# Kernel optimization log

Measured on AMD Instinct MI355X. Metric: run time of the kernel, lower is better.

The kernel has to match this reference:

```python
import jax, jax.numpy as jnp
import numpy as np

B, C, N, K, COUT = 4, 64, 8192, 16, 64
EPS = 1e-5  # BatchNorm1d default eps


def setup_inputs() -> dict:
    key = jax.random.key(0)
    k1, k2, k3 = jax.random.split(key, 3)
    x = jax.random.normal(k1, (B, C, N), dtype=jnp.float32)
    coords = jax.random.normal(k2, (B, 3, N), dtype=jnp.float32)
    # Linear(2C -> COUT) params
    W = jax.random.normal(k3, (2 * C, COUT), dtype=jnp.float32) * (1.0 / np.sqrt(2 * C))
    b = jnp.zeros((COUT,), dtype=jnp.float32)
    # BatchNorm1d affine params (train-mode batch stats, as in torch default)
    gamma = jnp.ones((COUT,), dtype=jnp.float32)
    beta = jnp.zeros((COUT,), dtype=jnp.float32)
    return {"x": x, "coords": coords, "W": W, "b": b, "gamma": gamma, "beta": beta}


def reference(x, coords, W, b, gamma, beta):
    k = min(K, max(N - 1, 1))
    # --- kNN in coordinate space (squared distances give same ordering as cdist) ---
    ct = jnp.swapaxes(coords, 1, 2)                      # (B, N, 3)
    sq = jnp.sum(ct * ct, axis=-1)                       # (B, N)
    d2 = sq[:, :, None] + sq[:, None, :] - 2.0 * jnp.einsum('bnd,bmd->bnm', ct, ct)
    _, idx = jax.lax.top_k(-d2, k + 1)                   # smallest k+1 distances
    idx = idx[:, :, 1:]                                  # drop self -> (B, N, k)
    # --- gather neighbor features ---
    xt = jnp.swapaxes(x, 1, 2)                           # (B, N, C)
    nb = jax.vmap(lambda f, i: f[i])(xt, idx)            # (B, N, k, C)
    center = jnp.broadcast_to(xt[:, :, None, :], nb.shape)
    edge = jnp.concatenate([center, nb - center], axis=-1)  # (B, N, k, 2C)
    # --- edge MLP: Linear -> BatchNorm1d (batch stats) -> ReLU ---
    h = jnp.einsum('bnkc,cd->bnkd', edge, W) + b         # (B, N, k, COUT)
    mean = jnp.mean(h, axis=(0, 1, 2))
    var = jnp.var(h, axis=(0, 1, 2))
    h = (h - mean) * jax.lax.rsqrt(var + EPS) * gamma + beta
    h = jax.nn.relu(h)
    # --- max-pool over k neighbors ---
    out = jnp.max(h, axis=2)                             # (B, N, COUT)
    return jnp.swapaxes(out, 1, 2)                       # (B, COUT, N)
```

## Files before the change

### kernel.cpp

```cpp
#include <hip/hip_runtime.h>


#define Bn 4
#define Cn 64
#define Nn 8192
#define Kn 16
#define TILE 512
#define CH 32

typedef unsigned long long ull;

__global__ __launch_bounds__(256) void transpose_kernel(const float* __restrict__ x,
                                                        float* __restrict__ xt) {
  __shared__ float tile[64][65];
  int bid = blockIdx.x;
  int b = bid >> 7;
  int n0 = (bid & 127) << 6;
  int tx = threadIdx.x & 63;
  int ty = threadIdx.x >> 6;
  for (int c = ty; c < 64; c += 4)
    tile[tx][c] = x[((size_t)b * 64 + c) * Nn + n0 + tx];
  __syncthreads();
  for (int r = ty; r < 64; r += 4)
    xt[((size_t)b * Nn + n0 + r) * 64 + tx] = tile[r][tx];
}


#define INSERT64(kv) do {                                     \
    ull _kk = (kv);                                           \
    bool _ci = _kk < ad[15];                                  \
    _Pragma("unroll")                                         \
    for (int _u = 15; _u >= 1; --_u) {                        \
      bool _cm = _kk < ad[_u - 1];                            \
      ull _nd = _cm ? ad[_u - 1] : _kk;                       \
      ad[_u] = _ci ? _nd : ad[_u];                            \
      _ci = _cm;                                              \
    }                                                         \
    ad[0] = _ci ? _kk : ad[0];                                \
    thr = ad[15];                                             \
  } while (0)

__global__ __launch_bounds__(256) void knn_kernel(const float* __restrict__ coords,
                                                  int* __restrict__ knn) {
  __shared__ float4 ctile[TILE];
  __shared__ unsigned fifo_d[CH * 256];
  __shared__ unsigned fifo_i[CH * 256];

  int bid = blockIdx.x;
  int b = bid >> 7;
  int q0 = (bid & 127) << 6;
  int tid = threadIdx.x;
  int q = tid & 63;
  int s = tid >> 6;
  int qg = q0 + q;

  const float* cb = coords + (size_t)b * 3 * Nn;
  float qx = cb[qg], qy = cb[Nn + qg], qz = cb[2 * Nn + qg];
  float qs = __fadd_rn(__fadd_rn(__fmul_rn(qx, qx), __fmul_rn(qy, qy)),
                       __fmul_rn(qz, qz));
  float qx2 = 2.f * qx, qy2 = 2.f * qy, qz2 = 2.f * qz;

  ull ad[16];
#pragma unroll
  for (int i = 0; i < 16; ++i) ad[i] = ~0ull;
  ull thr = ~0ull;
  unsigned thr_hi = 0xFFFFFFFFu;
  int bc = 0;

  for (int t = 0; t < Nn / TILE; ++t) {
    __syncthreads();
    for (int i = tid; i < TILE; i += 256) {
      int m = t * TILE + i;
      float cx = cb[m], cy = cb[Nn + m], cz = cb[2 * Nn + m];
      float cs = __fadd_rn(__fadd_rn(__fmul_rn(cx, cx), __fmul_rn(cy, cy)),
                           __fmul_rn(cz, cz));
      ctile[i] = make_float4(cx, cy, cz, cs);
    }
    __syncthreads();
    int jb = s * (TILE / 4);
    for (int c = 0; c < (TILE / 4) / CH; ++c) {
#pragma unroll 8
      for (int j = 0; j < CH; ++j) {
        int ji = jb + c * CH + j;
        float4 c4 = ctile[ji];
        float dot2 = __fadd_rn(__fadd_rn(__fmul_rn(qx2, c4.x), __fmul_rn(qy2, c4.y)),
                               __fmul_rn(qz2, c4.z));
        float d2 = __fsub_rn(__fadd_rn(qs, c4.w), dot2);
        int m = t * TILE + ji;
        unsigned bits = __float_as_uint(d2);
        if (bits <= thr_hi && m != qg) {
          fifo_d[bc * 256 + tid] = bits;
          fifo_i[bc * 256 + tid] = (unsigned)m;
          ++bc;
        }
      }
      for (int u = 0; u < bc; ++u) {
        ull kk = ((ull)fifo_d[u * 256 + tid] << 32) | fifo_i[u * 256 + tid];
        if (kk < thr) INSERT64(kk);
      }
      bc = 0;
      thr_hi = (unsigned)(thr >> 32);
    }
  }

  __syncthreads();
  if (s > 0) {
#pragma unroll
    for (int i = 0; i < 16; ++i) {
      int slot = ((((s - 1) << 4) + i) << 6) + q;
      fifo_d[slot] = (unsigned)(ad[i] >> 32);
      fifo_i[slot] = (unsigned)(ad[i] & 0xFFFFFFFFull);
    }
  }
  __syncthreads();
  if (s == 0) {
    for (int t = 0; t < 48; ++t) {
      int slot = (t << 6) + q;
      ull kk = ((ull)fifo_d[slot] << 32) | fifo_i[slot];
      if (kk < thr) INSERT64(kk);
    }
    int* op = knn + (size_t)(b * Nn + qg) * 16;
#pragma unroll
    for (int i = 0; i < 16; ++i) op[i] = (int)(ad[i] & 0xFFFFFFFFull);
  }
}

__global__ __launch_bounds__(256) void edge_kernel(
    const float* __restrict__ xt, const int* __restrict__ knn,
    const float* __restrict__ W, const float* __restrict__ bias,
    float* __restrict__ mnb, float* __restrict__ mxb,
    float* __restrict__ ps1, float* __restrict__ ps2) {
  __shared__ float dlds[4][16][64];
  __shared__ float clds[4][64];
  __shared__ float r1[4][64], r2[4][64];

  int tid = threadIdx.x;
  int l = tid & 63;
  int w = tid >> 6;

  float w1[64], w2[64];
#pragma unroll
  for (int c = 0; c < 64; ++c) {
    w1[c] = W[c * 64 + l];
    w2[c] = W[(64 + c) * 64 + l];
  }
  float bl = bias[l];
  float s1 = 0.f, s2 = 0.f;

  int wid = blockIdx.x * 4 + w;
  int nw = gridDim.x * 4;
  for (int p = wid; p < Bn * Nn; p += nw) {
    int bb = p >> 13;
    const float* xb = xt + (size_t)bb * Nn * 64;
    float ctr = xt[(size_t)p * 64 + l];
    clds[w][l] = ctr;
    const int* ip = knn + (size_t)p * 16;
#pragma unroll
    for (int j = 0; j < 16; ++j) {
      int nj = ip[j];
      dlds[w][j][l] = xb[(size_t)nj * 64 + l] - ctr;
    }
    __syncthreads();

    float cc = bl;
#pragma unroll
    for (int c = 0; c < 64; ++c) cc = fmaf(clds[w][c], w1[c], cc);

    float mn = 3.0e38f, mx = -3.0e38f;
#pragma unroll
    for (int k = 0; k < 16; ++k) {
      float h = cc;
#pragma unroll
      for (int c = 0; c < 64; ++c) h = fmaf(dlds[w][k][c], w2[c], h);
      mn = fminf(mn, h);
      mx = fmaxf(mx, h);
      s1 += h;
      s2 = fmaf(h, h, s2);
    }
    mnb[(size_t)p * 64 + l] = mn;
    mxb[(size_t)p * 64 + l] = mx;
    __syncthreads();
  }

  r1[w][l] = s1; r2[w][l] = s2;
  __syncthreads();
  if (w == 0) {
    float a = r1[0][l] + r1[1][l] + r1[2][l] + r1[3][l];
    float c2 = r2[0][l] + r2[1][l] + r2[2][l] + r2[3][l];
    ps1[blockIdx.x * 64 + l] = a;
    ps2[blockIdx.x * 64 + l] = c2;
  }
}

__global__ __launch_bounds__(256) void stats_kernel(const float* __restrict__ ps1,
                                                    const float* __restrict__ ps2,
                                                    float* __restrict__ stats) {
  __shared__ float r1[4][64], r2[4][64];
  int c = threadIdx.x & 63, g = threadIdx.x >> 6;
  float a = 0.f, b2 = 0.f;
  for (int i = g; i < 512; i += 4) { a += ps1[i * 64 + c]; b2 += ps2[i * 64 + c]; }
  r1[g][c] = a; r2[g][c] = b2;
  __syncthreads();
  if (g == 0) {
    float s1 = r1[0][c] + r1[1][c] + r1[2][c] + r1[3][c];
    float s2 = r2[0][c] + r2[1][c] + r2[2][c] + r2[3][c];
    const float invM = 1.f / 524288.f;
    float mean = s1 * invM;
    float var = s2 * invM - mean * mean;
    stats[c] = mean;
    stats[64 + c] = var;
  }
}

__global__ __launch_bounds__(256) void final_kernel(
    const float* __restrict__ mnb, const float* __restrict__ mxb,
    const float* __restrict__ stats, const float* __restrict__ gamma,
    const float* __restrict__ beta, float* __restrict__ out) {
  __shared__ float tile[64][65];
  int bid = blockIdx.x;
  int b = bid >> 7;
  int n0 = (bid & 127) << 6;
  int tx = threadIdx.x & 63, ty = threadIdx.x >> 6;
  float mean = stats[tx], var = stats[64 + tx];
  float sc = gamma[tx] * rsqrtf(var + 1e-5f);
  float sh = fmaf(-mean, sc, beta[tx]);
  for (int r = ty; r < 64; r += 4) {
    size_t off = ((size_t)(b * Nn + n0 + r)) * 64 + tx;
    float lo = fmaf(mnb[off], sc, sh);
    float hi = fmaf(mxb[off], sc, sh);
    tile[tx][r] = fmaxf(fmaxf(hi, lo), 0.f);
  }
  __syncthreads();
  for (int r = ty; r < 64; r += 4)
    out[((size_t)b * 64 + r) * Nn + n0 + tx] = tile[r][tx];
}

extern "C" void kernel_launch(void* const* d_in, const int* in_sizes, int n_in,
                              void* d_out, int out_size, void* d_ws, size_t ws_size,
                              hipStream_t stream) {
  const float* x      = (const float*)d_in[0];
  const float* coords = (const float*)d_in[1];
  const float* W      = (const float*)d_in[2];
  const float* bias   = (const float*)d_in[3];
  const float* gamma  = (const float*)d_in[4];
  const float* beta   = (const float*)d_in[5];
  float* out = (float*)d_out;

  char* ws = (char*)d_ws;
  float* xt    = (float*)ws;
  int*   knn   = (int*)(ws + 8388608);
  float* mnb   = (float*)(ws + 10485760);
  float* mxb   = (float*)(ws + 18874368);
  float* ps1   = (float*)(ws + 27262976);
  float* ps2   = (float*)(ws + 27394048);
  float* stats = (float*)(ws + 27525120);

  transpose_kernel<<<dim3(512), dim3(256), 0, stream>>>(x, xt);
  knn_kernel<<<dim3(512), dim3(256), 0, stream>>>(coords, knn);
  edge_kernel<<<dim3(512), dim3(256), 0, stream>>>(xt, knn, W, bias, mnb, mxb, ps1, ps2);
  stats_kernel<<<dim3(1), dim3(256), 0, stream>>>(ps1, ps2, stats);
  final_kernel<<<dim3(512), dim3(256), 0, stream>>>(mnb, mxb, stats, gamma, beta, out);
}
```

Baseline: 587.9 us.

## Restructure kNN with packed coords, 8 slices, bitmask candidate insertion

Coordinates and their squared norms are precomputed into a packed float4 buffer inside the transpose kernel. The buffer aliases the mnb workspace region, which is only written later by the edge kernel. The kNN kernel drops the shared-memory coordinate tiles and per-thread FIFOs and reads candidates straight from global/L2. It doubles to 8 slices (512 threads), builds a 32-bit candidate mask per chunk, and then recomputes and inserts the masked candidates in a wave-uniform loop. This removes LDS staging, block-wide syncs and FIFO traffic, at the cost of recomputing distances, more divergence in the insert loop, and a larger final merge (112 entries versus 48).

After: 653.4 us. +11.1%, slower.

```diff
diff --git a/kernel.cpp b/kernel.cpp
--- a/kernel.cpp
+++ b/kernel.cpp
@@ -5,13 +5,15 @@
 #define Cn 64
 #define Nn 8192
 #define Kn 16
-#define TILE 512
 #define CH 32
+#define NSL 8
 
 typedef unsigned long long ull;
 
 __global__ __launch_bounds__(256) void transpose_kernel(const float* __restrict__ x,
-                                                        float* __restrict__ xt) {
+                                                        const float* __restrict__ coords,
+                                                        float* __restrict__ xt,
+                                                        float4* __restrict__ cpack) {
   __shared__ float tile[64][65];
   int bid = blockIdx.x;
   int b = bid >> 7;
@@ -20,6 +22,14 @@
   int ty = threadIdx.x >> 6;
   for (int c = ty; c < 64; c += 4)
     tile[tx][c] = x[((size_t)b * 64 + c) * Nn + n0 + tx];
+  if (ty == 0) {
+    int n = n0 + tx;
+    const float* cb = coords + (size_t)b * 3 * Nn;
+    float cx = cb[n], cy = cb[Nn + n], cz = cb[2 * Nn + n];
+    float cs = __fadd_rn(__fadd_rn(__fmul_rn(cx, cx), __fmul_rn(cy, cy)),
+                         __fmul_rn(cz, cz));
+    cpack[(size_t)b * Nn + n] = make_float4(cx, cy, cz, cs);
+  }
   __syncthreads();
   for (int r = ty; r < 64; r += 4)
     xt[((size_t)b * Nn + n0 + r) * 64 + tx] = tile[r][tx];
@@ -40,11 +50,9 @@
     thr = ad[15];                                             \
   } while (0)
 
-__global__ __launch_bounds__(256) void knn_kernel(const float* __restrict__ coords,
+__global__ __launch_bounds__(512) void knn_kernel(const float4* __restrict__ cpack,
                                                   int* __restrict__ knn) {
-  __shared__ float4 ctile[TILE];
-  __shared__ unsigned fifo_d[CH * 256];
-  __shared__ unsigned fifo_i[CH * 256];
+  __shared__ ull mk[(NSL - 1) * 16][64];
 
   int bid = blockIdx.x;
   int b = bid >> 7;
@@ -54,69 +62,54 @@
   int s = tid >> 6;
   int qg = q0 + q;
 
-  const float* cb = coords + (size_t)b * 3 * Nn;
-  float qx = cb[qg], qy = cb[Nn + qg], qz = cb[2 * Nn + qg];
-  float qs = __fadd_rn(__fadd_rn(__fmul_rn(qx, qx), __fmul_rn(qy, qy)),
-                       __fmul_rn(qz, qz));
-  float qx2 = 2.f * qx, qy2 = 2.f * qy, qz2 = 2.f * qz;
+  const float4* cp = cpack + (size_t)b * Nn;
+  float4 qc = cp[qg];
+  float qs = qc.w;
+  float qx2 = 2.f * qc.x, qy2 = 2.f * qc.y, qz2 = 2.f * qc.z;
 
   ull ad[16];
 #pragma unroll
   for (int i = 0; i < 16; ++i) ad[i] = ~0ull;
   ull thr = ~0ull;
   unsigned thr_hi = 0xFFFFFFFFu;
-  int bc = 0;
-
-  for (int t = 0; t < Nn / TILE; ++t) {
-    __syncthreads();
-    for (int i = tid; i < TILE; i += 256) {
-      int m = t * TILE + i;
-      float cx = cb[m], cy = cb[Nn + m], cz = cb[2 * Nn + m];
-      float cs = __fadd_rn(__fadd_rn(__fmul_rn(cx, cx), __fmul_rn(cy, cy)),
-                           __fmul_rn(cz, cz));
-      ctile[i] = make_float4(cx, cy, cz, cs);
-    }
-    __syncthreads();
-    int jb = s * (TILE / 4);
-    for (int c = 0; c < (TILE / 4) / CH; ++c) {
+
+  for (int c = 0; c < Nn / (NSL * CH); ++c) {
+    int base = c * (NSL * CH) + s * CH;
+    const float4* cpb = cp + base;
+    unsigned mask = 0;
 #pragma unroll 8
-      for (int j = 0; j < CH; ++j) {
-        int ji = jb + c * CH + j;
-        float4 c4 = ctile[ji];
+    for (int j = 0; j < CH; ++j) {
+      float4 c4 = cpb[j];
+      float dot2 = __fadd_rn(__fadd_rn(__fmul_rn(qx2, c4.x), __fmul_rn(qy2, c4.y)),
+                             __fmul_rn(qz2, c4.z));
+      float d2 = __fsub_rn(__fadd_rn(qs, c4.w), dot2);
+      mask |= (__float_as_uint(d2) <= thr_hi) ? (1u << j) : 0u;
+    }
+    unsigned sj = (unsigned)(qg - base);
+    if (sj < 32u) mask &= ~(1u << sj);
+    while (__any(mask)) {
+      if (mask) {
+        int j = __ffs(mask) - 1;
+        mask &= (mask - 1);
+        float4 c4 = cpb[j];
         float dot2 = __fadd_rn(__fadd_rn(__fmul_rn(qx2, c4.x), __fmul_rn(qy2, c4.y)),
                                __fmul_rn(qz2, c4.z));
         float d2 = __fsub_rn(__fadd_rn(qs, c4.w), dot2);
-        int m = t * TILE + ji;
-        unsigned bits = __float_as_uint(d2);
-        if (bits <= thr_hi && m != qg) {
-          fifo_d[bc * 256 + tid] = bits;
-          fifo_i[bc * 256 + tid] = (unsigned)m;
-          ++bc;
-        }
+        ull key = ((ull)__float_as_uint(d2) << 32) | (unsigned)(base + j);
+        if (key < thr) INSERT64(key);
       }
-      for (int u = 0; u < bc; ++u) {
-        ull kk = ((ull)fifo_d[u * 256 + tid] << 32) | fifo_i[u * 256 + tid];
-        if (kk < thr) INSERT64(kk);
-      }
-      bc = 0;
-      thr_hi = (unsigned)(thr >> 32);
-    }
-  }
-
-  __syncthreads();
+    }
+    thr_hi = (unsigned)(thr >> 32);
+  }
+
   if (s > 0) {
 #pragma unroll
-    for (int i = 0; i < 16; ++i) {
-      int slot = ((((s - 1) << 4) + i) << 6) + q;
-      fifo_d[slot] = (unsigned)(ad[i] >> 32);
-      fifo_i[slot] = (unsigned)(ad[i] & 0xFFFFFFFFull);
-    }
+    for (int i = 0; i < 16; ++i) mk[(s - 1) * 16 + i][q] = ad[i];
   }
   __syncthreads();
   if (s == 0) {
-    for (int t = 0; t < 48; ++t) {
-      int slot = (t << 6) + q;
-      ull kk = ((ull)fifo_d[slot] << 32) | fifo_i[slot];
+    for (int t = 0; t < (NSL - 1) * 16; ++t) {
+      ull kk = mk[t][q];
       if (kk < thr) INSERT64(kk);
     }
     int* op = knn + (size_t)(b * Nn + qg) * 16;
@@ -247,16 +240,17 @@
   float* out = (float*)d_out;
 
   char* ws = (char*)d_ws;
-  float* xt    = (float*)ws;
-  int*   knn   = (int*)(ws + 8388608);
-  float* mnb   = (float*)(ws + 10485760);
-  float* mxb   = (float*)(ws + 18874368);
-  float* ps1   = (float*)(ws + 27262976);
-  float* ps2   = (float*)(ws + 27394048);
-  float* stats = (float*)(ws + 27525120);
-
-  transpose_kernel<<<dim3(512), dim3(256), 0, stream>>>(x, xt);
-  knn_kernel<<<dim3(512), dim3(256), 0, stream>>>(coords, knn);
+  float*  xt    = (float*)ws;
+  int*    knn   = (int*)(ws + 8388608);
+  float*  mnb   = (float*)(ws + 10485760);
+  float4* cpack = (float4*)(ws + 10485760);
+  float*  mxb   = (float*)(ws + 18874368);
+  float*  ps1   = (float*)(ws + 27262976);
+  float*  ps2   = (float*)(ws + 27394048);
+  float*  stats = (float*)(ws + 27525120);
+
+  transpose_kernel<<<dim3(512), dim3(256), 0, stream>>>(x, coords, xt, cpack);
+  knn_kernel<<<dim3(512), dim3(512), 0, stream>>>(cpack, knn);
   edge_kernel<<<dim3(512), dim3(256), 0, stream>>>(xt, knn, W, bias, mnb, mxb, ps1, ps2);
   stats_kernel<<<dim3(1), dim3(256), 0, stream>>>(ps1, ps2, stats);
   final_kernel<<<dim3(512), dim3(256), 0, stream>>>(mnb, mxb, stats, gamma, beta, out);
```
